# Performance work log

Measured on AMD Instinct MI355X. Metric: run time of the kernel, lower is better.

The kernel has to match this reference:

```python
import jax, jax.numpy as jnp
import numpy as np

N_NODES = 100000
N_EDGES = 1600000
IN_CH = 128
HEADS = 4
OUT_CH = 32


def setup_inputs() -> dict:
    key = jax.random.key(0)
    k1, k2, k3, k4 = jax.random.split(key, 4)
    x = jax.random.normal(k1, (N_NODES, IN_CH), dtype=jnp.float32)
    edge_index = jax.random.randint(k2, (2, N_EDGES), 0, N_NODES, dtype=jnp.int64)
    # linear weight stored as [in, heads*out] so projection is x @ W
    W = jax.random.normal(k3, (IN_CH, HEADS * OUT_CH), dtype=jnp.float32) * (1.0 / np.sqrt(IN_CH))
    att = jax.random.normal(k4, (HEADS, OUT_CH), dtype=jnp.float32)
    return {"x": x, "edge_index": edge_index, "W": W, "att": att}


def reference(x, edge_index, W, att):
    N = x.shape[0]
    row, col = edge_index[0], edge_index[1]
    # project and split heads: [N, H, C]
    projected = (x @ W).reshape(N, HEADS, OUT_CH)
    src = projected[row]                      # [E, H, C]
    dst = projected[col]                      # [E, H, C]
    scores = jnp.tanh(src + dst)              # [E, H, C]
    scores = jnp.einsum('ehc,hc->eh', scores, att)  # [E, H]
    # stabilize by global per-head max over edges, then exp
    scores = jnp.exp(scores - jnp.max(scores, axis=0, keepdims=True))
    # scatter-add over destination nodes
    out = jax.ops.segment_sum(src * scores[:, :, None], col, num_segments=N)  # [N, H, C]
    normalizer = jax.ops.segment_sum(scores, col, num_segments=N)             # [N, H]
    out = out / jnp.maximum(normalizer, 1e-12)[:, :, None]
    return out.reshape(N, HEADS * OUT_CH)
```

## Files before the change

### kernel.cpp

```cpp
#include <hip/hip_runtime.h>
#include <hip/hip_fp16.h>

#define IN_CH 128
#define HEADS 4
#define OUT_CH 32
#define HC 128
#define SCORE_BLOCKS 4096
#define CHUNK 2048
#define BW_SHIFT 9
#define BW (1 << BW_SHIFT)

__device__ __forceinline__ unsigned flip_f32(float x) {
  unsigned u = __float_as_uint(x);
  return (u & 0x80000000u) ? ~u : (u | 0x80000000u);
}
__device__ __forceinline__ float unflip_f32(unsigned k) {
  unsigned u = (k & 0x80000000u) ? (k ^ 0x80000000u) : ~k;
  return __uint_as_float(u);
}
__device__ __forceinline__ float fast_tanh(float x) {
#if __has_builtin(__builtin_amdgcn_exp2f)
  const float t = __builtin_amdgcn_exp2f(x * 2.8853900817779268f);
#else
  const float t = __expf(2.f * x);
#endif
#if __has_builtin(__builtin_amdgcn_rcpf)
  return 1.f - 2.f * __builtin_amdgcn_rcpf(t + 1.f);
#else
  return 1.f - 2.f / (t + 1.f);
#endif
}

__device__ __forceinline__ float4 ldh4(const __half* p) {
  const uint2 u = *(const uint2*)p;
  const float2 a = __half22float2(*(const __half2*)&u.x);
  const float2 b = __half22float2(*(const __half2*)&u.y);
  return make_float4(a.x, a.y, b.x, b.y);
}

__global__ __launch_bounds__(256) void gemm_xW(const float* __restrict__ x,
                                               const float* __restrict__ W,
                                               __half* __restrict__ proj, int N,
                                               const int* __restrict__ ecol,
                                               int* __restrict__ hist, int E) {
  __shared__ float xs[128][68];
  __shared__ float ws[128][68];
  const int tid = threadIdx.x;
  const int rowblk = blockIdx.x >> 1;
  const int colblk = blockIdx.x & 1;
  const int row0 = rowblk * 64;
  const int col0 = colblk * 64;

  {
    const int k = tid >> 1;
    const int c0 = (tid & 1) * 32;
    const float4* src = (const float4*)(W + (size_t)k * HC + col0 + c0);
#pragma unroll
    for (int i = 0; i < 8; ++i) *(float4*)&ws[k][c0 + i * 4] = src[i];
  }
  {
    const int r = tid >> 2;
    const int k0 = (tid & 3) * 32;
    const int grow = row0 + r;
    const bool valid = grow < N;
    const float4* src = (const float4*)(x + (size_t)grow * IN_CH + k0);
#pragma unroll
    for (int i = 0; i < 8; ++i) {
      float4 v = valid ? src[i] : make_float4(0.f, 0.f, 0.f, 0.f);
      const int k = k0 + i * 4;
      xs[k][r] = v.x; xs[k + 1][r] = v.y; xs[k + 2][r] = v.z; xs[k + 3][r] = v.w;
    }
  }
  __syncthreads();

  const int cg2 = tid & 15;
  const int rg = tid >> 4;
  float acc[4][4];
#pragma unroll
  for (int r = 0; r < 4; ++r)
#pragma unroll
    for (int c = 0; c < 4; ++c) acc[r][c] = 0.f;

#pragma unroll 8
  for (int k = 0; k < 128; ++k) {
    const float4 a = *(const float4*)&xs[k][rg * 4];
    const float4 b = *(const float4*)&ws[k][cg2 * 4];
    const float xv[4] = {a.x, a.y, a.z, a.w};
    const float wv[4] = {b.x, b.y, b.z, b.w};
#pragma unroll
    for (int r = 0; r < 4; ++r)
#pragma unroll
      for (int c = 0; c < 4; ++c) acc[r][c] += xv[r] * wv[c];
  }

#pragma unroll
  for (int r = 0; r < 4; ++r) {
    const int grow = row0 + rg * 4 + r;
    if (grow < N) {
      const __half2 p0 = __floats2half2_rn(acc[r][0], acc[r][1]);
      const __half2 p1 = __floats2half2_rn(acc[r][2], acc[r][3]);
      uint2 w;
      w.x = *(const unsigned*)&p0;
      w.y = *(const unsigned*)&p1;
      *(uint2*)(proj + (size_t)grow * HC + col0 + cg2 * 4) = w;
    }
  }

  if (hist) {
    const int ehb = (E + gridDim.x - 1) / gridDim.x;
    const int estart = blockIdx.x * ehb;
    const int eend = min(estart + ehb, E);
    for (int e = estart + tid; e < eend; e += 256) atomicAdd(&hist[ecol[e]], 1);
  }
}

__device__ __forceinline__ int block_scan_excl(int tsum, int* ls, int tid, int* total) {
  ls[tid] = tsum;
  __syncthreads();
  for (int off = 1; off < 256; off <<= 1) {
    int v = (tid >= off) ? ls[tid - off] : 0;
    __syncthreads();
    ls[tid] += v;
    __syncthreads();
  }
  *total = ls[255];
  return ls[tid] - tsum;
}

__global__ __launch_bounds__(256) void k_scan(const int* __restrict__ hist,
                                              int* __restrict__ sums,
                                              unsigned* __restrict__ flags,
                                              int* __restrict__ starts,
                                              int nb, int nc) {
  __shared__ int ls[256];
  const int tid = threadIdx.x;
  const int bid = blockIdx.x;
  const int base = bid * CHUNK + tid * 8;
  int h[8];
  int t = 0;
#pragma unroll
  for (int j = 0; j < 8; ++j) {
    const int i = base + j;
    h[j] = (i < nb) ? hist[i] : 0;
    t += h[j];
  }
  int total;
  const int excl = block_scan_excl(t, ls, tid, &total);
  if (tid == 0) {
    __hip_atomic_store(&sums[bid], total, __ATOMIC_RELAXED, __HIP_MEMORY_SCOPE_AGENT);
    __hip_atomic_store(&flags[bid], 1u, __ATOMIC_RELEASE, __HIP_MEMORY_SCOPE_AGENT);
  }
  int my = 0;
  if (tid < bid) {
    while (__hip_atomic_load(&flags[tid], __ATOMIC_ACQUIRE, __HIP_MEMORY_SCOPE_AGENT) == 0u) {}
    my = __hip_atomic_load(&sums[tid], __ATOMIC_RELAXED, __HIP_MEMORY_SCOPE_AGENT);
  }
  __syncthreads();
  ls[tid] = my;
  __syncthreads();
  for (int off = 128; off >= 1; off >>= 1) {
    if (tid < off) ls[tid] += ls[tid + off];
    __syncthreads();
  }
  const int cbase = ls[0];
  int run = cbase + excl;
#pragma unroll
  for (int j = 0; j < 8; ++j) {
    const int i = base + j;
    if (i < nb) { starts[i] = run; run += h[j]; }
  }
  if (bid == nc - 1 && tid == 0) starts[nb] = cbase + total;
}

__global__ __launch_bounds__(256) void bucket_split(const int* __restrict__ erow,
                                                    const int* __restrict__ ecol,
                                                    const int* __restrict__ starts,
                                                    int* __restrict__ bcnt,
                                                    int2* __restrict__ aux,
                                                    int E, int NB) {
  __shared__ int cnt[1024];
  __shared__ int base[1024];
  const int tid = threadIdx.x;
  for (int b = tid; b < NB; b += 256) cnt[b] = 0;
  __syncthreads();
  const int e0 = blockIdx.x * 2048;
  int rows[8], cols[8], loc[8];
#pragma unroll
  for (int j = 0; j < 8; ++j) {
    const int e = e0 + j * 256 + tid;
    if (e < E) {
      cols[j] = ecol[e];
      rows[j] = erow[e];
      loc[j] = atomicAdd(&cnt[cols[j] >> BW_SHIFT], 1);
    } else {
      loc[j] = -1;
    }
  }
  __syncthreads();
  for (int b = tid; b < NB; b += 256) {
    const int c = cnt[b];
    base[b] = (c ? atomicAdd(&bcnt[b], c) : 0) + starts[b << BW_SHIFT];
  }
  __syncthreads();
#pragma unroll
  for (int j = 0; j < 8; ++j) {
    if (loc[j] >= 0) {
      const int b = cols[j] >> BW_SHIFT;
      aux[base[b] + loc[j]] = make_int2(rows[j] * HC, cols[j]);
    }
  }
}

__global__ __launch_bounds__(256) void bucket_place(const int2* __restrict__ aux,
                                                    const int* __restrict__ starts,
                                                    int* __restrict__ rc, int N) {
  __shared__ int lcnt[BW];
  const int tid = threadIdx.x;
  const int n0 = blockIdx.x << BW_SHIFT;
  const int n1 = min(n0 + BW, N);
  for (int i = tid; i < BW; i += 256) lcnt[i] = 0;
  __syncthreads();
  const int e0 = starts[n0];
  const int e1 = starts[n1];
  for (int i = e0 + tid; i < e1; i += 256) {
    const int2 pr = aux[i];
    const int r = atomicAdd(&lcnt[pr.y & (BW - 1)], 1);
    rc[starts[pr.y] + r] = pr.x;
  }
}

__global__ __launch_bounds__(256) void fused_apply(const __half* __restrict__ proj,
                                                   const int* __restrict__ rc,
                                                   const int* __restrict__ starts,
                                                   const float* __restrict__ att,
                                                   float* __restrict__ out,
                                                   float* __restrict__ den,
                                                   unsigned* __restrict__ headmax_u, int N) {
  __shared__ unsigned blkmax[HEADS];
  const int tid = threadIdx.x;
  if (tid < HEADS) blkmax[tid] = 0u;
  __syncthreads();
  const int lane = tid & 63;
  const int half = lane >> 5;
  const int l = lane & 31;
  const int c0 = l * 4;
  const int head = l >> 3;
  const int n = blockIdx.x * 4 + (tid >> 6);
  float lm = -3.0e38f;

  if (n < N) {
    const float4 a4 = ((const float4*)att)[l];
    float M0 = fabsf(a4.x) + fabsf(a4.y) + fabsf(a4.z) + fabsf(a4.w);
    M0 += __shfl_xor(M0, 4, 64);
    M0 += __shfl_xor(M0, 2, 64);
    M0 += __shfl_xor(M0, 1, 64);
    const float4 d4 = ldh4(proj + (size_t)n * HC + c0);
    const int beg = __builtin_amdgcn_readfirstlane(starts[n]);
    const int end = __builtin_amdgcn_readfirstlane(starts[n + 1]);

    float ax = 0.f, ay = 0.f, az = 0.f, aw = 0.f, dsum = 0.f;
    int i = beg;
    for (; i + 8 <= end; i += 8) {
      const int r0 = rc[i + half];
      const int r1 = rc[i + 2 + half];
      const int r2 = rc[i + 4 + half];
      const int r3 = rc[i + 6 + half];
      const float4 s0 = ldh4(proj + r0 + c0);
      const float4 s1 = ldh4(proj + r1 + c0);
      const float4 s2 = ldh4(proj + r2 + c0);
      const float4 s3 = ldh4(proj + r3 + c0);
      float p0 = fast_tanh(s0.x + d4.x) * a4.x + fast_tanh(s0.y + d4.y) * a4.y
               + fast_tanh(s0.z + d4.z) * a4.z + fast_tanh(s0.w + d4.w) * a4.w;
      float p1 = fast_tanh(s1.x + d4.x) * a4.x + fast_tanh(s1.y + d4.y) * a4.y
               + fast_tanh(s1.z + d4.z) * a4.z + fast_tanh(s1.w + d4.w) * a4.w;
      float p2 = fast_tanh(s2.x + d4.x) * a4.x + fast_tanh(s2.y + d4.y) * a4.y
               + fast_tanh(s2.z + d4.z) * a4.z + fast_tanh(s2.w + d4.w) * a4.w;
      float p3 = fast_tanh(s3.x + d4.x) * a4.x + fast_tanh(s3.y + d4.y) * a4.y
               + fast_tanh(s3.z + d4.z) * a4.z + fast_tanh(s3.w + d4.w) * a4.w;
      p0 += __shfl_xor(p0, 4, 64);  p1 += __shfl_xor(p1, 4, 64);
      p2 += __shfl_xor(p2, 4, 64);  p3 += __shfl_xor(p3, 4, 64);
      p0 += __shfl_xor(p0, 2, 64);  p1 += __shfl_xor(p1, 2, 64);
      p2 += __shfl_xor(p2, 2, 64);  p3 += __shfl_xor(p3, 2, 64);
      p0 += __shfl_xor(p0, 1, 64);  p1 += __shfl_xor(p1, 1, 64);
      p2 += __shfl_xor(p2, 1, 64);  p3 += __shfl_xor(p3, 1, 64);
      lm = fmaxf(lm, fmaxf(fmaxf(p0, p1), fmaxf(p2, p3)));
      const float e0 = __expf(p0 - M0);
      const float e1 = __expf(p1 - M0);
      const float e2 = __expf(p2 - M0);
      const float e3 = __expf(p3 - M0);
      ax += s0.x * e0 + s1.x * e1 + s2.x * e2 + s3.x * e3;
      ay += s0.y * e0 + s1.y * e1 + s2.y * e2 + s3.y * e3;
      az += s0.z * e0 + s1.z * e1 + s2.z * e2 + s3.z * e3;
      aw += s0.w * e0 + s1.w * e1 + s2.w * e2 + s3.w * e3;
      dsum += (e0 + e1) + (e2 + e3);
    }
    if (i + 4 <= end) {
      const int r0 = rc[i + half];
      const int r1 = rc[i + 2 + half];
      const float4 s0 = ldh4(proj + r0 + c0);
      const float4 s1 = ldh4(proj + r1 + c0);
      float p0 = fast_tanh(s0.x + d4.x) * a4.x + fast_tanh(s0.y + d4.y) * a4.y
               + fast_tanh(s0.z + d4.z) * a4.z + fast_tanh(s0.w + d4.w) * a4.w;
      float p1 = fast_tanh(s1.x + d4.x) * a4.x + fast_tanh(s1.y + d4.y) * a4.y
               + fast_tanh(s1.z + d4.z) * a4.z + fast_tanh(s1.w + d4.w) * a4.w;
      p0 += __shfl_xor(p0, 4, 64);  p1 += __shfl_xor(p1, 4, 64);
      p0 += __shfl_xor(p0, 2, 64);  p1 += __shfl_xor(p1, 2, 64);
      p0 += __shfl_xor(p0, 1, 64);  p1 += __shfl_xor(p1, 1, 64);
      lm = fmaxf(lm, fmaxf(p0, p1));
      const float e0 = __expf(p0 - M0);
      const float e1 = __expf(p1 - M0);
      ax += s0.x * e0 + s1.x * e1;
      ay += s0.y * e0 + s1.y * e1;
      az += s0.z * e0 + s1.z * e1;
      aw += s0.w * e0 + s1.w * e1;
      dsum += e0 + e1;
      i += 4;
    }
    for (; i < end; i += 2) {
      const int idx = i + half;
      const bool valid = idx < end;
      const int row = rc[valid ? idx : i];
      const float4 s4 = ldh4(proj + row + c0);
      float p = fast_tanh(s4.x + d4.x) * a4.x
              + fast_tanh(s4.y + d4.y) * a4.y
              + fast_tanh(s4.z + d4.z) * a4.z
              + fast_tanh(s4.w + d4.w) * a4.w;
      p += __shfl_xor(p, 4, 64);
      p += __shfl_xor(p, 2, 64);
      p += __shfl_xor(p, 1, 64);
      if (!valid) p = -3.0e38f;
      lm = fmaxf(lm, p);
      const float e = __expf(p - M0);
      ax += s4.x * e; ay += s4.y * e; az += s4.z * e; aw += s4.w * e;
      dsum += e;
    }
    dsum += __shfl_xor(dsum, 32, 64);
    ax += __shfl_xor(ax, 32, 64);
    ay += __shfl_xor(ay, 32, 64);
    az += __shfl_xor(az, 32, 64);
    aw += __shfl_xor(aw, 32, 64);
    lm = fmaxf(lm, __shfl_xor(lm, 32, 64));
    if (half == 0) {
      const float inv = 1.f / fmaxf(dsum, 1e-38f);
      *(float4*)(out + (size_t)n * HC + c0) =
          make_float4(ax * inv, ay * inv, az * inv, aw * inv);
      if ((l & 7) == 0) den[n * HEADS + head] = dsum;
      if ((l & 7) == 0) atomicMax(&blkmax[head], flip_f32(lm));
    }
  }
  __syncthreads();
  if (tid < HEADS) {
    const unsigned v = blkmax[tid];
    if (v > headmax_u[tid]) atomicMax(&headmax_u[tid], v);
  }
}

__global__ __launch_bounds__(256) void fix_clamp(float* __restrict__ out,
                                                 const float* __restrict__ den,
                                                 const unsigned* __restrict__ headmax_u,
                                                 const float* __restrict__ att, int N) {
  const int t = blockIdx.x * 256 + threadIdx.x;
  if (t >= N * HEADS) return;
  const int n = t >> 2;
  const int h = t & 3;
  float M0 = 0.f;
#pragma unroll
  for (int c = 0; c < OUT_CH; ++c) M0 += fabsf(att[h * OUT_CH + c]);
  const float Mt = unflip_f32(headmax_u[h]);
  const float f = den[t] * __expf(M0 - Mt);
  if (f < 1e-12f) {
    const float s = f * 1e12f;
    float4* p = (float4*)(out + (size_t)n * HC + h * OUT_CH);
#pragma unroll
    for (int j = 0; j < 8; ++j) {
      float4 v = p[j];
      v.x *= s; v.y *= s; v.z *= s; v.w *= s;
      p[j] = v;
    }
  }
}

__global__ __launch_bounds__(256) void reduce_corr(const unsigned* __restrict__ blockmax,
                                                   const float* __restrict__ att,
                                                   float* __restrict__ corr, int nblk) {
  __shared__ unsigned sm[HEADS];
  const int tid = threadIdx.x;
  if (tid < HEADS) sm[tid] = 0u;
  __syncthreads();
  const int h = tid & 3;
  unsigned k = 0u;
  for (int i = tid >> 2; i < nblk; i += 64) k = max(k, blockmax[i * HEADS + h]);
  atomicMax(&sm[h], k);
  __syncthreads();
  if (tid < HEADS) {
    const float Mt = unflip_f32(sm[tid]);
    float M0 = 0.f;
#pragma unroll
    for (int c = 0; c < OUT_CH; ++c) M0 += fabsf(att[tid * OUT_CH + c]);
    corr[tid] = __expf(M0 - Mt);
    corr[4 + tid] = Mt;
  }
}

__global__ __launch_bounds__(256) void score_max(const __half* __restrict__ proj,
                                                 const int* __restrict__ erow,
                                                 const int* __restrict__ ecol,
                                                 const float* __restrict__ att,
                                                 unsigned* __restrict__ blockmax, int E) {
  __shared__ unsigned blkmax[HEADS];
  const int tid = threadIdx.x;
  if (tid < HEADS) blkmax[tid] = 0u;
  __syncthreads();
  const int lane = tid & 63;
  const int wid = tid >> 6;
  const float a0 = att[lane];
  const float a1 = att[lane + 64];
  float lmA = -3.0e38f, lmB = -3.0e38f;
  const int stride = SCORE_BLOCKS * 16;

  for (int base = (blockIdx.x * 4 + wid) * 4; base < E; base += stride) {
    const int bu = __builtin_amdgcn_readfirstlane(base);
    const int lim = min(bu + 4, E);
    for (int e = bu; e < lim; ++e) {
      const int r0 = erow[e], c0 = ecol[e];
      const __half* ps = proj + (size_t)r0 * HC;
      const __half* pd = proj + (size_t)c0 * HC;
      float pA = fast_tanh(__half2float(ps[lane]) + __half2float(pd[lane])) * a0;
      float pB = fast_tanh(__half2float(ps[lane + 64]) + __half2float(pd[lane + 64])) * a1;
#pragma unroll
      for (int m = 16; m >= 1; m >>= 1) {
        pA += __shfl_xor(pA, m, 64);
        pB += __shfl_xor(pB, m, 64);
      }
      lmA = fmaxf(lmA, pA);
      lmB = fmaxf(lmB, pB);
    }
  }
  if ((lane & 31) == 0) {
    const int hh = lane >> 5;
    atomicMax(&blkmax[hh], flip_f32(lmA));
    atomicMax(&blkmax[hh + 2], flip_f32(lmB));
  }
  __syncthreads();
  if (tid < HEADS) blockmax[blockIdx.x * HEADS + tid] = blkmax[tid];
}

__global__ __launch_bounds__(256) void edge_apply_fb(const __half* __restrict__ proj,
                                                     const int* __restrict__ erow,
                                                     const int* __restrict__ ecol,
                                                     const float* __restrict__ att,
                                                     const float* __restrict__ headmax,
                                                     float* __restrict__ out,
                                                     float* __restrict__ norm, int E) {
  const int tid = threadIdx.x;
  const int e = blockIdx.x * 2 + (tid >> 7);
  if (e >= E) return;
  const int ch = tid & 127;
  const int h = ch >> 5;
  const float M = headmax[h];
  const int row = erow[e];
  const int col = ecol[e];
  const float sv = __half2float(proj[(size_t)row * HC + ch]);
  const float dv = __half2float(proj[(size_t)col * HC + ch]);
  float p = fast_tanh(sv + dv) * att[ch];
#pragma unroll
  for (int m = 16; m >= 1; m >>= 1) p += __shfl_xor(p, m, 64);
  const float w = __expf(p - M);
  unsafeAtomicAdd(&out[(size_t)col * HC + ch], sv * w);
  if ((ch & 31) == 0) unsafeAtomicAdd(&norm[(size_t)col * HEADS + h], w);
}

__global__ __launch_bounds__(256) void finalize_fb(float* __restrict__ out,
                                                   const float* __restrict__ norm, int N) {
  const int idx = blockIdx.x * blockDim.x + threadIdx.x;
  const int total = N * (HC / 4);
  if (idx >= total) return;
  const int base = idx * 4;
  const int node = base >> 7;
  const int h = (base >> 5) & 3;
  const float inv = 1.f / fmaxf(norm[node * HEADS + h], 1e-12f);
  float4 v = ((float4*)out)[idx];
  v.x *= inv; v.y *= inv; v.z *= inv; v.w *= inv;
  ((float4*)out)[idx] = v;
}

extern "C" void kernel_launch(void* const* d_in, const int* in_sizes, int n_in,
                              void* d_out, int out_size, void* d_ws, size_t ws_size,
                              hipStream_t stream) {
  const float* x    = (const float*)d_in[0];
  const int*   eidx = (const int*)d_in[1];
  const float* W    = (const float*)d_in[2];
  const float* att  = (const float*)d_in[3];
  float* out = (float*)d_out;

  const int N = in_sizes[0] / IN_CH;
  const int E = in_sizes[1] / 2;
  const int nb = N;
  const int nc = (nb + CHUNK - 1) / CHUNK;
  const int NB = (N + BW - 1) >> BW_SHIFT;
  const int ngemm = ((N + 63) / 64) * 2;

  char* p = (char*)d_ws;
  __half* proj = (__half*)p;  p += (((size_t)N * HC * 2 + 15) & ~15ull);
  int* rc = (int*)p;        p += (((size_t)E * 4 + 15) & ~15ull);
  float* den = (float*)p;   p += (((size_t)N * HEADS * 4 + 15) & ~15ull);
  int* hist = (int*)p;      p += (((size_t)(nb + 4 + 256 + NB) * 4 + 15) & ~15ull);
  int* starts = (int*)p;    p += (((size_t)(nb + 1) * 4 + 15) & ~15ull);
  int2* aux = (int2*)p;     p += (((size_t)E * 8 + 15) & ~15ull);
  int* sums = (int*)p;      p += 1024;
  unsigned* headmax_u = (unsigned*)(hist + nb);
  unsigned* flags = (unsigned*)(hist + nb + 4);
  int* bcnt = hist + nb + 4 + 256;
  const size_t need_full = (size_t)(p - (char*)d_ws);
  const bool full = (ws_size >= need_full) && (nc <= 256) && (NB <= 1024);

  if (full) {
    hipMemsetAsync(hist, 0, (size_t)(nb + 4 + 256 + NB) * sizeof(int), stream);
    gemm_xW<<<ngemm, 256, 0, stream>>>(x, W, proj, N, eidx + E, hist, E);
    k_scan<<<nc, 256, 0, stream>>>(hist, sums, flags, starts, nb, nc);
    bucket_split<<<(E + 2047) / 2048, 256, 0, stream>>>(eidx, eidx + E, starts,
                                                        bcnt, aux, E, NB);
    bucket_place<<<NB, 256, 0, stream>>>(aux, starts, rc, N);
    fused_apply<<<(N + 3) / 4, 256, 0, stream>>>(proj, rc, starts, att, out, den,
                                                 headmax_u, N);
    fix_clamp<<<(N * HEADS + 255) / 256, 256, 0, stream>>>(out, den, headmax_u, att, N);
  } else {
    gemm_xW<<<ngemm, 256, 0, stream>>>(x, W, proj, N, nullptr, nullptr, 0);
    unsigned* bm = (unsigned*)((char*)d_ws + (((size_t)N * HC * 2 + 15) & ~15ull));
    float* cr = (float*)(bm + SCORE_BLOCKS * HEADS);
    float* norm = cr + 8;
    hipMemsetAsync(out, 0, (size_t)out_size * sizeof(float), stream);
    hipMemsetAsync(norm, 0, (size_t)N * HEADS * sizeof(float), stream);
    score_max<<<SCORE_BLOCKS, 256, 0, stream>>>(proj, eidx, eidx + E, att, bm, E);
    reduce_corr<<<1, 256, 0, stream>>>(bm, att, cr, SCORE_BLOCKS);
    edge_apply_fb<<<(E + 1) / 2, 256, 0, stream>>>(proj, eidx, eidx + E, att, cr + 4, out, norm, E);
    finalize_fb<<<(N * (HC / 4) + 255) / 256, 256, 0, stream>>>(out, norm, N);
  }
}
```

Before: 402.6 us.

## Build CSR via bucket histogram and fuse tanh-dot into single reciprocal

The per-node global histogram and multi-block decoupled scan are replaced by a per-bucket histogram accumulated in shared memory inside the GEMM kernel, a single-block bucket scan, and per-bucket node counting and scanning inside bucket_place. This removes 1.6M global atomics and the large scan kernel. Separately, the four tanh terms of the attention dot product are combined algebraically over a common denominator, so one reciprocal replaces four. That can lose precision or overflow when the exp terms get large.

```diff
diff --git a/kernel.cpp b/kernel.cpp
--- a/kernel.cpp
+++ b/kernel.cpp
@@ -6,7 +6,6 @@
 #define OUT_CH 32
 #define HC 128
 #define SCORE_BLOCKS 4096
-#define CHUNK 2048
 #define BW_SHIFT 9
 #define BW (1 << BW_SHIFT)
 
@@ -18,17 +17,36 @@
   unsigned u = (k & 0x80000000u) ? (k ^ 0x80000000u) : ~k;
   return __uint_as_float(u);
 }
+__device__ __forceinline__ float fexp2(float x) {
+#if __has_builtin(__builtin_amdgcn_exp2f)
+  return __builtin_amdgcn_exp2f(x);
+#else
+  return exp2f(x);
+#endif
+}
+__device__ __forceinline__ float frcp(float x) {
+#if __has_builtin(__builtin_amdgcn_rcpf)
+  return __builtin_amdgcn_rcpf(x);
+#else
+  return 1.f / x;
+#endif
+}
 __device__ __forceinline__ float fast_tanh(float x) {
-#if __has_builtin(__builtin_amdgcn_exp2f)
-  const float t = __builtin_amdgcn_exp2f(x * 2.8853900817779268f);
-#else
-  const float t = __expf(2.f * x);
-#endif
-#if __has_builtin(__builtin_amdgcn_rcpf)
-  return 1.f - 2.f * __builtin_amdgcn_rcpf(t + 1.f);
-#else
-  return 1.f - 2.f / (t + 1.f);
-#endif
+  return 1.f - 2.f * frcp(fexp2(x * 2.8853900817779268f) + 1.f);
+}
+
+__device__ __forceinline__ float att_tanh_dot(float4 s, float4 d, float4 a, float A) {
+  const float K = 2.8853900817779268f;
+  const float t0 = fexp2((s.x + d.x) * K) + 1.f;
+  const float t1 = fexp2((s.y + d.y) * K) + 1.f;
+  const float t2 = fexp2((s.z + d.z) * K) + 1.f;
+  const float t3 = fexp2((s.w + d.w) * K) + 1.f;
+  const float p01 = t0 * t1, p23 = t2 * t3;
+  const float R = frcp(p01 * p23);
+  const float n01 = a.x * t1 + a.y * t0;
+  const float n23 = a.z * t3 + a.w * t2;
+  const float num = n01 * p23 + n23 * p01;
+  return A - 2.f * num * R;
 }
 
 __device__ __forceinline__ float4 ldh4(const __half* p) {
@@ -42,9 +60,10 @@
                                                const float* __restrict__ W,
                                                __half* __restrict__ proj, int N,
                                                const int* __restrict__ ecol,
-                                               int* __restrict__ hist, int E) {
+                                               int* __restrict__ bcnt0, int E, int NB) {
   __shared__ float xs[128][68];
   __shared__ float ws[128][68];
+  __shared__ int cnt[1024];
   const int tid = threadIdx.x;
   const int rowblk = blockIdx.x >> 1;
   const int colblk = blockIdx.x & 1;
@@ -70,6 +89,9 @@
       const int k = k0 + i * 4;
       xs[k][r] = v.x; xs[k + 1][r] = v.y; xs[k + 2][r] = v.z; xs[k + 3][r] = v.w;
     }
+  }
+  if (bcnt0) {
+    for (int b = tid; b < NB; b += 256) cnt[b] = 0;
   }
   __syncthreads();
 
@@ -106,11 +128,17 @@
     }
   }
 
-  if (hist) {
+  if (bcnt0) {
     const int ehb = (E + gridDim.x - 1) / gridDim.x;
     const int estart = blockIdx.x * ehb;
     const int eend = min(estart + ehb, E);
-    for (int e = estart + tid; e < eend; e += 256) atomicAdd(&hist[ecol[e]], 1);
+    for (int e = estart + tid; e < eend; e += 256)
+      atomicAdd(&cnt[ecol[e] >> BW_SHIFT], 1);
+    __syncthreads();
+    for (int b = tid; b < NB; b += 256) {
+      const int c = cnt[b];
+      if (c) atomicAdd(&bcnt0[b], c);
+    }
   }
 }
 
@@ -127,54 +155,31 @@
   return ls[tid] - tsum;
 }
 
-__global__ __launch_bounds__(256) void k_scan(const int* __restrict__ hist,
-                                              int* __restrict__ sums,
-                                              unsigned* __restrict__ flags,
-                                              int* __restrict__ starts,
-                                              int nb, int nc) {
+__global__ __launch_bounds__(256) void bucket_scan(const int* __restrict__ bcnt0,
+                                                   int* __restrict__ bstarts, int NB) {
   __shared__ int ls[256];
   const int tid = threadIdx.x;
-  const int bid = blockIdx.x;
-  const int base = bid * CHUNK + tid * 8;
-  int h[8];
+  int v[4];
   int t = 0;
 #pragma unroll
-  for (int j = 0; j < 8; ++j) {
-    const int i = base + j;
-    h[j] = (i < nb) ? hist[i] : 0;
-    t += h[j];
+  for (int j = 0; j < 4; ++j) {
+    const int idx = tid * 4 + j;
+    v[j] = (idx < NB) ? bcnt0[idx] : 0;
+    t += v[j];
   }
   int total;
-  const int excl = block_scan_excl(t, ls, tid, &total);
-  if (tid == 0) {
-    __hip_atomic_store(&sums[bid], total, __ATOMIC_RELAXED, __HIP_MEMORY_SCOPE_AGENT);
-    __hip_atomic_store(&flags[bid], 1u, __ATOMIC_RELEASE, __HIP_MEMORY_SCOPE_AGENT);
-  }
-  int my = 0;
-  if (tid < bid) {
-    while (__hip_atomic_load(&flags[tid], __ATOMIC_ACQUIRE, __HIP_MEMORY_SCOPE_AGENT) == 0u) {}
-    my = __hip_atomic_load(&sums[tid], __ATOMIC_RELAXED, __HIP_MEMORY_SCOPE_AGENT);
-  }
-  __syncthreads();
-  ls[tid] = my;
-  __syncthreads();
-  for (int off = 128; off >= 1; off >>= 1) {
-    if (tid < off) ls[tid] += ls[tid + off];
-    __syncthreads();
-  }
-  const int cbase = ls[0];
-  int run = cbase + excl;
-#pragma unroll
-  for (int j = 0; j < 8; ++j) {
-    const int i = base + j;
-    if (i < nb) { starts[i] = run; run += h[j]; }
-  }
-  if (bid == nc - 1 && tid == 0) starts[nb] = cbase + total;
+  int run = block_scan_excl(t, ls, tid, &total);
+#pragma unroll
+  for (int j = 0; j < 4; ++j) {
+    const int idx = tid * 4 + j;
+    if (idx < NB) { bstarts[idx] = run; run += v[j]; }
+  }
+  if (tid == 0) bstarts[NB] = total;
 }
 
 __global__ __launch_bounds__(256) void bucket_split(const int* __restrict__ erow,
                                                     const int* __restrict__ ecol,
-                                                    const int* __restrict__ starts,
+                                                    const int* __restrict__ bstarts,
                                                     int* __restrict__ bcnt,
                                                     int2* __restrict__ aux,
                                                     int E, int NB) {
@@ -199,7 +204,7 @@
   __syncthreads();
   for (int b = tid; b < NB; b += 256) {
     const int c = cnt[b];
-    base[b] = (c ? atomicAdd(&bcnt[b], c) : 0) + starts[b << BW_SHIFT];
+    base[b] = (c ? atomicAdd(&bcnt[b], c) : 0) + bstarts[b];
   }
   __syncthreads();
 #pragma unroll
@@ -212,20 +217,37 @@
 }
 
 __global__ __launch_bounds__(256) void bucket_place(const int2* __restrict__ aux,
-                                                    const int* __restrict__ starts,
-                                                    int* __restrict__ rc, int N) {
+                                                    const int* __restrict__ bstarts,
+                                                    int* __restrict__ starts,
+                                                    int* __restrict__ rc, int N, int NB) {
   __shared__ int lcnt[BW];
-  const int tid = threadIdx.x;
-  const int n0 = blockIdx.x << BW_SHIFT;
+  __shared__ int ls[256];
+  const int tid = threadIdx.x;
+  const int b = blockIdx.x;
+  const int n0 = b << BW_SHIFT;
   const int n1 = min(n0 + BW, N);
+  const int e0 = bstarts[b];
+  const int e1 = bstarts[b + 1];
   for (int i = tid; i < BW; i += 256) lcnt[i] = 0;
   __syncthreads();
-  const int e0 = starts[n0];
-  const int e1 = starts[n1];
+  for (int i = e0 + tid; i < e1; i += 256)
+    atomicAdd(&lcnt[aux[i].y & (BW - 1)], 1);
+  __syncthreads();
+  const int c0 = lcnt[2 * tid];
+  const int c1 = lcnt[2 * tid + 1];
+  int total;
+  const int excl = block_scan_excl(c0 + c1, ls, tid, &total);
+  const int n = n0 + 2 * tid;
+  if (n < n1) starts[n] = e0 + excl;
+  if (n + 1 < n1) starts[n + 1] = e0 + excl + c0;
+  lcnt[2 * tid] = e0 + excl;
+  lcnt[2 * tid + 1] = e0 + excl + c0;
+  if (b == NB - 1 && tid == 0) starts[N] = e1;
+  __syncthreads();
   for (int i = e0 + tid; i < e1; i += 256) {
     const int2 pr = aux[i];
     const int r = atomicAdd(&lcnt[pr.y & (BW - 1)], 1);
-    rc[starts[pr.y] + r] = pr.x;
+    rc[r] = pr.x;
   }
 }
 
@@ -250,6 +272,7 @@
 
   if (n < N) {
     const float4 a4 = ((const float4*)att)[l];
+    const float A = ((a4.x + a4.y) + (a4.z + a4.w));
     float M0 = fabsf(a4.x) + fabsf(a4.y) + fabsf(a4.z) + fabsf(a4.w);
     M0 += __shfl_xor(M0, 4, 64);
     M0 += __shfl_xor(M0, 2, 64);
@@ -269,14 +292,10 @@
       const float4 s1 = ldh4(proj + r1 + c0);
       const float4 s2 = ldh4(proj + r2 + c0);
       const float4 s3 = ldh4(proj + r3 + c0);
-      float p0 = fast_tanh(s0.x + d4.x) * a4.x + fast_tanh(s0.y + d4.y) * a4.y
-               + fast_tanh(s0.z + d4.z) * a4.z + fast_tanh(s0.w + d4.w) * a4.w;
-      float p1 = fast_tanh(s1.x + d4.x) * a4.x + fast_tanh(s1.y + d4.y) * a4.y
-               + fast_tanh(s1.z + d4.z) * a4.z + fast_tanh(s1.w + d4.w) * a4.w;
-      float p2 = fast_tanh(s2.x + d4.x) * a4.x + fast_tanh(s2.y + d4.y) * a4.y
-               + fast_tanh(s2.z + d4.z) * a4.z + fast_tanh(s2.w + d4.w) * a4.w;
-      float p3 = fast_tanh(s3.x + d4.x) * a4.x + fast_tanh(s3.y + d4.y) * a4.y
-               + fast_tanh(s3.z + d4.z) * a4.z + fast_tanh(s3.w + d4.w) * a4.w;
+      float p0 = att_tanh_dot(s0, d4, a4, A);
+      float p1 = att_tanh_dot(s1, d4, a4, A);
+      float p2 = att_tanh_dot(s2, d4, a4, A);
+      float p3 = att_tanh_dot(s3, d4, a4, A);
       p0 += __shfl_xor(p0, 4, 64);  p1 += __shfl_xor(p1, 4, 64);
       p2 += __shfl_xor(p2, 4, 64);  p3 += __shfl_xor(p3, 4, 64);
       p0 += __shfl_xor(p0, 2, 64);  p1 += __shfl_xor(p1, 2, 64);
@@ -299,10 +318,8 @@
       const int r1 = rc[i + 2 + half];
       const float4 s0 = ldh4(proj + r0 + c0);
       const float4 s1 = ldh4(proj + r1 + c0);
-      float p0 = fast_tanh(s0.x + d4.x) * a4.x + fast_tanh(s0.y + d4.y) * a4.y
-               + fast_tanh(s0.z + d4.z) * a4.z + fast_tanh(s0.w + d4.w) * a4.w;
-      float p1 = fast_tanh(s1.x + d4.x) * a4.x + fast_tanh(s1.y + d4.y) * a4.y
-               + fast_tanh(s1.z + d4.z) * a4.z + fast_tanh(s1.w + d4.w) * a4.w;
+      float p0 = att_tanh_dot(s0, d4, a4, A);
+      float p1 = att_tanh_dot(s1, d4, a4, A);
       p0 += __shfl_xor(p0, 4, 64);  p1 += __shfl_xor(p1, 4, 64);
       p0 += __shfl_xor(p0, 2, 64);  p1 += __shfl_xor(p1, 2, 64);
       p0 += __shfl_xor(p0, 1, 64);  p1 += __shfl_xor(p1, 1, 64);
@@ -321,10 +338,7 @@
       const bool valid = idx < end;
       const int row = rc[valid ? idx : i];
       const float4 s4 = ldh4(proj + row + c0);
-      float p = fast_tanh(s4.x + d4.x) * a4.x
-              + fast_tanh(s4.y + d4.y) * a4.y
-              + fast_tanh(s4.z + d4.z) * a4.z
-              + fast_tanh(s4.w + d4.w) * a4.w;
+      float p = att_tanh_dot(s4, d4, a4, A);
       p += __shfl_xor(p, 4, 64);
       p += __shfl_xor(p, 2, 64);
       p += __shfl_xor(p, 1, 64);
@@ -495,8 +509,6 @@
 
   const int N = in_sizes[0] / IN_CH;
   const int E = in_sizes[1] / 2;
-  const int nb = N;
-  const int nc = (nb + CHUNK - 1) / CHUNK;
   const int NB = (N + BW - 1) >> BW_SHIFT;
   const int ngemm = ((N + 63) / 64) * 2;
 
@@ -504,28 +516,28 @@
   __half* proj = (__half*)p;  p += (((size_t)N * HC * 2 + 15) & ~15ull);
   int* rc = (int*)p;        p += (((size_t)E * 4 + 15) & ~15ull);
   float* den = (float*)p;   p += (((size_t)N * HEADS * 4 + 15) & ~15ull);
-  int* hist = (int*)p;      p += (((size_t)(nb + 4 + 256 + NB) * 4 + 15) & ~15ull);
-  int* starts = (int*)p;    p += (((size_t)(nb + 1) * 4 + 15) & ~15ull);
+  int* small = (int*)p;     p += (((size_t)(2 * NB + 4 + NB + 1) * 4 + 15) & ~15ull);
+  int* starts = (int*)p;    p += (((size_t)(N + 1) * 4 + 15) & ~15ull);
   int2* aux = (int2*)p;     p += (((size_t)E * 8 + 15) & ~15ull);
-  int* sums = (int*)p;      p += 1024;
-  unsigned* headmax_u = (unsigned*)(hist + nb);
-  unsigned* flags = (unsigned*)(hist + nb + 4);
-  int* bcnt = hist + nb + 4 + 256;
+  int* bcnt0 = small;
+  int* bcnt = small + NB;
+  unsigned* headmax_u = (unsigned*)(small + 2 * NB);
+  int* bstarts = small + 2 * NB + 4;
   const size_t need_full = (size_t)(p - (char*)d_ws);
-  const bool full = (ws_size >= need_full) && (nc <= 256) && (NB <= 1024);
+  const bool full = (ws_size >= need_full) && (NB <= 1024);
 
   if (full) {
-    hipMemsetAsync(hist, 0, (size_t)(nb + 4 + 256 + NB) * sizeof(int), stream);
-    gemm_xW<<<ngemm, 256, 0, stream>>>(x, W, proj, N, eidx + E, hist, E);
-    k_scan<<<nc, 256, 0, stream>>>(hist, sums, flags, starts, nb, nc);
-    bucket_split<<<(E + 2047) / 2048, 256, 0, stream>>>(eidx, eidx + E, starts,
+    hipMemsetAsync(small, 0, (size_t)(2 * NB + 4) * sizeof(int), stream);
+    gemm_xW<<<ngemm, 256, 0, stream>>>(x, W, proj, N, eidx + E, bcnt0, E, NB);
+    bucket_scan<<<1, 256, 0, stream>>>(bcnt0, bstarts, NB);
+    bucket_split<<<(E + 2047) / 2048, 256, 0, stream>>>(eidx, eidx + E, bstarts,
                                                         bcnt, aux, E, NB);
-    bucket_place<<<NB, 256, 0, stream>>>(aux, starts, rc, N);
+    bucket_place<<<NB, 256, 0, stream>>>(aux, bstarts, starts, rc, N, NB);
     fused_apply<<<(N + 3) / 4, 256, 0, stream>>>(proj, rc, starts, att, out, den,
                                                  headmax_u, N);
     fix_clamp<<<(N * HEADS + 255) / 256, 256, 0, stream>>>(out, den, headmax_u, att, N);
   } else {
-    gemm_xW<<<ngemm, 256, 0, stream>>>(x, W, proj, N, nullptr, nullptr, 0);
+    gemm_xW<<<ngemm, 256, 0, stream>>>(x, W, proj, N, nullptr, nullptr, 0, 0);
     unsigned* bm = (unsigned*)((char*)d_ws + (((size_t)N * HC * 2 + 15) & ~15ull));
     float* cr = (float*)(bm + SCORE_BLOCKS * HEADS);
     float* norm = cr + 8;
```

Measured after the change: 379.3 us. 1.06x faster.
